# Performance work log

Measured on AMD Instinct MI355X. Metric: run time of the kernel, lower is better.

## Reference

```python
import jax, jax.numpy as jnp
import numpy as np
from jax import lax

# static config
P = 16          # patch_len
S = 8           # stride_base
MAX_OFF = 4.0


def setup_inputs() -> dict:
    key = jax.random.key(0)
    ks = jax.random.split(key, 7)
    B, L, N, A, D = 64, 512, 64, 64, 256
    x = jax.random.normal(ks[0], (B, L, N), dtype=jnp.float32)
    conv_w = jax.random.normal(ks[1], (32, N, 3), dtype=jnp.float32) * 0.05
    conv_b = jnp.zeros((32,), dtype=jnp.float32)
    lin_w = jax.random.normal(ks[2], (A, 32), dtype=jnp.float32) * 0.1
    lin_b = jnp.zeros((A,), dtype=jnp.float32)
    wp_w = jax.random.normal(ks[3], (D, P), dtype=jnp.float32) * 0.1
    wp_b = jnp.zeros((D,), dtype=jnp.float32)
    return {"x": x, "conv_w": conv_w, "conv_b": conv_b,
            "lin_w": lin_w, "lin_b": lin_b, "wp_w": wp_w, "wp_b": wp_b}


def _forward(x, conv_w, conv_b, lin_w, lin_b, wp_w, wp_b):
    B, L, N = x.shape
    A = lin_w.shape[0]
    D = wp_w.shape[0]
    z = jnp.transpose(x, (0, 2, 1))  # (B, N, L) -- channels = series

    # offset head: Conv1d(N->32, k=3, pad=1) -> ReLU -> global avg pool -> Linear(32->A)
    h = lax.conv_general_dilated(z, conv_w, window_strides=(1,),
                                 padding=[(1, 1)],
                                 dimension_numbers=("NCH", "OIH", "NCH"))
    h = jax.nn.relu(h + conv_b[None, :, None])      # (B, 32, L)
    pooled = jnp.mean(h, axis=-1)                    # (B, 32)
    delta = MAX_OFF * jnp.tanh(pooled @ lin_w.T + lin_b)  # (B, A)

    # sampling positions: anchor + offset + centered patch index, clamped to [0, L-1]
    anchors = jnp.arange(A, dtype=jnp.float32) * S
    pidx = jnp.arange(P, dtype=jnp.float32) - (P - 1) / 2.0
    xs = anchors[None, :, None] + delta[:, :, None] + pidx[None, None, :]  # (B, A, P)
    xs = jnp.clip(xs, 0.0, float(L - 1))

    # 1D bilinear gather (equivalent to grid_sample with y=0, border pad, align_corners=True)
    i0 = jnp.floor(xs).astype(jnp.int32)
    f = xs - i0.astype(xs.dtype)                     # (B, A, P)
    i1 = jnp.minimum(i0 + 1, L - 1)
    gather = jax.vmap(lambda zb, ib: zb[:, ib])      # (N,L),(A,P) -> (N,A,P)
    g0 = gather(z, i0)                               # (B, N, A, P)
    g1 = gather(z, i1)
    samp = g0 * (1.0 - f)[:, None] + g1 * f[:, None]  # (B, N, A, P)

    # patch projection W_P: (P -> D)
    out = jnp.einsum("bnap,dp->bnad", samp, wp_w) + wp_b  # (B, N, A, D)
    return out.reshape(B * N, A, D)


def reference(x, conv_w, conv_b, lin_w, lin_b, wp_w, wp_b):
    return _forward(x, conv_w, conv_b, lin_w, lin_b, wp_w, wp_b)
```

## Files before the change

kernel.cpp:

```cpp
#include <hip/hip_runtime.h>
#include <hip/hip_bf16.h>
#include <cmath>

#define BB 64
#define LL 512
#define NN 64
#define AA 64
#define PP 16
#define DD 256
#define MAX_OFF 4.0f
#define STRIDE_S 8

typedef __attribute__((ext_vector_type(8))) short short8_t;
typedef __attribute__((ext_vector_type(4))) float float4_t;

static __device__ __forceinline__ unsigned f2bf(float x) {
    union { float f; unsigned u; } v; v.f = x;
    return (v.u + 0x7FFFu + ((v.u >> 16) & 1u)) >> 16;
}

__global__ __launch_bounds__(256) void conv_pool_kernel(
    const float* __restrict__ x,
    const float* __restrict__ conv_w,
    const float* __restrict__ conv_b,
    float* __restrict__ pool_partial)
{
    const int c = blockIdx.x;
    const int b = blockIdx.y;
    const int t = threadIdx.x;

    __shared__ float4 wl[3 * 16 * 32];
    __shared__ float  xl[66 * 64];
    __shared__ float  red[8][32];

    for (int idx = t; idx < 1536; idx += 256) {
        int o  = idx & 31;
        int nv = (idx >> 5) & 15;
        int k  = idx >> 9;
        float4 v;
        v.x = conv_w[(o * 64 + nv * 4 + 0) * 3 + k];
        v.y = conv_w[(o * 64 + nv * 4 + 1) * 3 + k];
        v.z = conv_w[(o * 64 + nv * 4 + 2) * 3 + k];
        v.w = conv_w[(o * 64 + nv * 4 + 3) * 3 + k];
        wl[idx] = v;
    }

    const int base_row = c * 64 - 1;
    for (int idx = t; idx < 66 * 16; idx += 256) {
        int j  = idx >> 4;
        int nv = idx & 15;
        int row = base_row + j;
        float4 v = make_float4(0.f, 0.f, 0.f, 0.f);
        if (row >= 0 && row < LL)
            v = *reinterpret_cast<const float4*>(&x[((size_t)b * LL + row) * NN + nv * 4]);
        *reinterpret_cast<float4*>(&xl[j * 64 + nv * 4]) = v;
    }
    __syncthreads();

    const int o  = t & 31;
    const int lg = t >> 5;

    float s[8];
#pragma unroll
    for (int j = 0; j < 8; ++j) s[j] = 0.f;

#pragma unroll
    for (int nv = 0; nv < 16; ++nv) {
        float4 xv[10];
#pragma unroll
        for (int j = 0; j < 10; ++j)
            xv[j] = *reinterpret_cast<const float4*>(&xl[(lg * 8 + j) * 64 + nv * 4]);
#pragma unroll
        for (int k = 0; k < 3; ++k) {
            float4 w4 = wl[(k * 16 + nv) * 32 + o];
#pragma unroll
            for (int j = 0; j < 8; ++j) {
                s[j] = fmaf(xv[j + k].x, w4.x, s[j]);
                s[j] = fmaf(xv[j + k].y, w4.y, s[j]);
                s[j] = fmaf(xv[j + k].z, w4.z, s[j]);
                s[j] = fmaf(xv[j + k].w, w4.w, s[j]);
            }
        }
    }

    const float cb = conv_b[o];
    float part = 0.f;
#pragma unroll
    for (int j = 0; j < 8; ++j) part += fmaxf(s[j] + cb, 0.f);
    red[lg][o] = part;
    __syncthreads();

    if (t < 32) {
        float sum = 0.f;
#pragma unroll
        for (int g = 0; g < 8; ++g) sum += red[g][t];
        pool_partial[((size_t)b * 8 + c) * 32 + t] = sum;
    }
}

__global__ __launch_bounds__(64) void delta_kernel(
    const float* __restrict__ pool_partial,
    const float* __restrict__ lin_w,
    const float* __restrict__ lin_b,
    const float* __restrict__ wp_w,
    float* __restrict__ delta,
    unsigned short* __restrict__ wp16)
{
    const int b = blockIdx.x;
    const int t = threadIdx.x;
    __shared__ float pooled[32];

    if (t < 32) {
        float s = 0.f;
#pragma unroll
        for (int c = 0; c < 8; ++c) s += pool_partial[((size_t)b * 8 + c) * 32 + t];
        pooled[t] = s * (1.0f / 512.0f);
    }
    __syncthreads();

    float s = lin_b[t];
#pragma unroll
    for (int o = 0; o < 32; ++o) s = fmaf(pooled[o], lin_w[t * 32 + o], s);
    delta[b * AA + t] = MAX_OFF * tanhf(s);

    if (b == 0) {
        const float4* w4 = reinterpret_cast<const float4*>(wp_w);
        uint2* o2 = reinterpret_cast<uint2*>(wp16);
#pragma unroll
        for (int i = 0; i < 16; ++i) {
            float4 v = w4[i * 64 + t];
            uint2 pk;
            pk.x = f2bf(v.x) | (f2bf(v.y) << 16);
            pk.y = f2bf(v.z) | (f2bf(v.w) << 16);
            o2[i * 64 + t] = pk;
        }
    }
}

#define XR_STRIDE 68
#define SA_ST     24

__global__ __launch_bounds__(256) void patch_proj_kernel(
    const float* __restrict__ x,
    const unsigned short* __restrict__ wp16,
    const float* __restrict__ wp_b,
    const float* __restrict__ delta,
    float* __restrict__ out)
{
    const int a = blockIdx.x;
    const int b = blockIdx.y;
    const int t = threadIdx.x;
    const int lane = t & 63;
    const int w  = t >> 6;
    const int lg = lane >> 4;
    const int lr = lane & 15;

    __shared__ float          xr[17 * XR_STRIDE];
    __shared__ unsigned short sampA[64 * SA_ST];

    const float dlt  = delta[b * AA + a];
    const float base = (float)(a * STRIDE_S) - 7.5f + dlt;
    const int   r0   = (int)floorf(base);

    for (int idx = t; idx < 17 * 16; idx += 256) {
        int j  = idx >> 4;
        int nv = idx & 15;
        int row = max(0, min(LL - 1, r0 + j));
        float4 v = *reinterpret_cast<const float4*>(&x[((size_t)b * LL + row) * NN + nv * 4]);
        *reinterpret_cast<float4*>(&xr[j * XR_STRIDE + nv * 4]) = v;
    }

    short8_t afrag[4];
    float4_t acc[4][4];
    const short8_t zero8 = {0, 0, 0, 0, 0, 0, 0, 0};
#pragma unroll
    for (int i = 0; i < 4; ++i) {
        const int d = w * 64 + i * 16 + lr;
        short8_t v = *reinterpret_cast<const short8_t*>(&wp16[d * 16 + (lg & 1) * 8]);
        afrag[i] = (lg < 2) ? v : zero8;
        float4 bv = *reinterpret_cast<const float4*>(&wp_b[w * 64 + i * 16 + lg * 4]);
        float4_t c4 = {bv.x, bv.y, bv.z, bv.w};
#pragma unroll
        for (int s = 0; s < 4; ++s) acc[s][i] = c4;
    }
    __syncthreads();

    {
        const int pp  = t & 7;
        const int nr0 = t >> 3;
        float f_[2]; int j0_[2], j1_[2];
#pragma unroll
        for (int q = 0; q < 2; ++q) {
            int p = pp * 2 + q;
            float xs = base + (float)p;
            xs = fminf(fmaxf(xs, 0.f), (float)(LL - 1));
            int i0 = (int)floorf(xs);
            f_[q]  = xs - (float)i0;
            j0_[q] = i0 - r0;
            j1_[q] = min(i0 + 1, LL - 1) - r0;
        }
#pragma unroll
        for (int h = 0; h < 2; ++h) {
            int n = nr0 + 32 * h;
            unsigned pk = 0;
#pragma unroll
            for (int q = 0; q < 2; ++q) {
                float g0 = xr[j0_[q] * XR_STRIDE + n];
                float g1 = xr[j1_[q] * XR_STRIDE + n];
                float s  = g0 + f_[q] * (g1 - g0);
                pk |= f2bf(s) << (16 * q);
            }
            *reinterpret_cast<unsigned*>(&sampA[n * SA_ST + pp * 2]) = pk;
        }
    }
    __syncthreads();

    short8_t bfrag[4];
#pragma unroll
    for (int s = 0; s < 4; ++s)
        bfrag[s] = *reinterpret_cast<const short8_t*>(
            &sampA[(s * 16 + lr) * SA_ST + (lg & 1) * 8]);

#pragma unroll
    for (int s = 0; s < 4; ++s)
#pragma unroll
        for (int i = 0; i < 4; ++i)
            acc[s][i] = __builtin_amdgcn_mfma_f32_16x16x32_bf16(
                afrag[i], bfrag[s], acc[s][i], 0, 0, 0);

    const size_t ob = (((size_t)b * NN) * AA + a) * DD + w * 64 + lg * 4;
#pragma unroll
    for (int s = 0; s < 4; ++s) {
        const int n = s * 16 + lr;
        const size_t rb = ob + (size_t)n * (AA * DD);
#pragma unroll
        for (int i = 0; i < 4; ++i)
            *reinterpret_cast<float4_t*>(&out[rb + i * 16]) = acc[s][i];
    }
}

extern "C" void kernel_launch(void* const* d_in, const int* in_sizes, int n_in,
                              void* d_out, int out_size, void* d_ws, size_t ws_size,
                              hipStream_t stream)
{
    const float* x      = (const float*)d_in[0];
    const float* conv_w = (const float*)d_in[1];
    const float* conv_b = (const float*)d_in[2];
    const float* lin_w  = (const float*)d_in[3];
    const float* lin_b  = (const float*)d_in[4];
    const float* wp_w   = (const float*)d_in[5];
    const float* wp_b   = (const float*)d_in[6];
    float* out = (float*)d_out;

    float* pool_partial = (float*)d_ws;
    float* delta        = pool_partial + 16384;
    unsigned short* wp16 = (unsigned short*)(delta + 4096);

    conv_pool_kernel<<<dim3(8, BB), 256, 0, stream>>>(x, conv_w, conv_b, pool_partial);
    delta_kernel<<<BB, 64, 0, stream>>>(pool_partial, lin_w, lin_b, wp_w, delta, wp16);
    patch_proj_kernel<<<dim3(AA, BB), 256, 0, stream>>>(x, wp16, wp_b, delta, out);
}
```

Baseline: 65.52 us.

## Fuse delta computation into patch projection and process four anchors per block

Removes the separate delta kernel: each patch-projection block now reduces the pooled partials, computes tanh offsets for its anchors, and converts wp_w to bf16 in registers. Each block handles four anchors, sharing one larger x window (49 rows) and the weight fragments across them, with a quarter of the blocks. This drops a kernel launch and its dependency gap and amortises setup per block. The cost is redundant pooled/offset and weight-conversion work in every block, plus less parallelism. The 49-row window assumes offsets stay within ±4, which MAX_OFF guarantees.

```diff
diff --git a/kernel.cpp b/kernel.cpp
--- a/kernel.cpp
+++ b/kernel.cpp
@@ -98,144 +98,148 @@
     }
 }
 
-__global__ __launch_bounds__(64) void delta_kernel(
+#define AGRP 4
+#define XROWS 49
+#define XR_STRIDE 68
+#define SA_ST 24
+
+__global__ __launch_bounds__(256) void patch_proj_kernel(
+    const float* __restrict__ x,
+    const float* __restrict__ wp_w,
+    const float* __restrict__ wp_b,
     const float* __restrict__ pool_partial,
     const float* __restrict__ lin_w,
     const float* __restrict__ lin_b,
-    const float* __restrict__ wp_w,
-    float* __restrict__ delta,
-    unsigned short* __restrict__ wp16)
-{
-    const int b = blockIdx.x;
-    const int t = threadIdx.x;
-    __shared__ float pooled[32];
-
-    if (t < 32) {
-        float s = 0.f;
-#pragma unroll
-        for (int c = 0; c < 8; ++c) s += pool_partial[((size_t)b * 8 + c) * 32 + t];
-        pooled[t] = s * (1.0f / 512.0f);
-    }
-    __syncthreads();
-
-    float s = lin_b[t];
-#pragma unroll
-    for (int o = 0; o < 32; ++o) s = fmaf(pooled[o], lin_w[t * 32 + o], s);
-    delta[b * AA + t] = MAX_OFF * tanhf(s);
-
-    if (b == 0) {
-        const float4* w4 = reinterpret_cast<const float4*>(wp_w);
-        uint2* o2 = reinterpret_cast<uint2*>(wp16);
-#pragma unroll
-        for (int i = 0; i < 16; ++i) {
-            float4 v = w4[i * 64 + t];
-            uint2 pk;
-            pk.x = f2bf(v.x) | (f2bf(v.y) << 16);
-            pk.y = f2bf(v.z) | (f2bf(v.w) << 16);
-            o2[i * 64 + t] = pk;
-        }
-    }
-}
-
-#define XR_STRIDE 68
-#define SA_ST     24
-
-__global__ __launch_bounds__(256) void patch_proj_kernel(
-    const float* __restrict__ x,
-    const unsigned short* __restrict__ wp16,
-    const float* __restrict__ wp_b,
-    const float* __restrict__ delta,
     float* __restrict__ out)
 {
-    const int a = blockIdx.x;
-    const int b = blockIdx.y;
-    const int t = threadIdx.x;
+    const int a0 = blockIdx.x * AGRP;
+    const int b  = blockIdx.y;
+    const int t  = threadIdx.x;
     const int lane = t & 63;
     const int w  = t >> 6;
     const int lg = lane >> 4;
     const int lr = lane & 15;
 
-    __shared__ float          xr[17 * XR_STRIDE];
-    __shared__ unsigned short sampA[64 * SA_ST];
-
-    const float dlt  = delta[b * AA + a];
-    const float base = (float)(a * STRIDE_S) - 7.5f + dlt;
-    const int   r0   = (int)floorf(base);
-
-    for (int idx = t; idx < 17 * 16; idx += 256) {
+    __shared__ float          xr[XROWS * XR_STRIDE];
+    __shared__ unsigned short sampA[AGRP * 64 * SA_ST];
+    __shared__ float          pooled[32];
+    __shared__ float          bases[AGRP];
+
+    const int r_lo = a0 * 8 - 12;
+
+    for (int idx = t; idx < XROWS * 16; idx += 256) {
         int j  = idx >> 4;
         int nv = idx & 15;
-        int row = max(0, min(LL - 1, r0 + j));
+        int row = max(0, min(LL - 1, r_lo + j));
         float4 v = *reinterpret_cast<const float4*>(&x[((size_t)b * LL + row) * NN + nv * 4]);
         *reinterpret_cast<float4*>(&xr[j * XR_STRIDE + nv * 4]) = v;
     }
-
-    short8_t afrag[4];
-    float4_t acc[4][4];
-    const short8_t zero8 = {0, 0, 0, 0, 0, 0, 0, 0};
-#pragma unroll
-    for (int i = 0; i < 4; ++i) {
-        const int d = w * 64 + i * 16 + lr;
-        short8_t v = *reinterpret_cast<const short8_t*>(&wp16[d * 16 + (lg & 1) * 8]);
-        afrag[i] = (lg < 2) ? v : zero8;
-        float4 bv = *reinterpret_cast<const float4*>(&wp_b[w * 64 + i * 16 + lg * 4]);
-        float4_t c4 = {bv.x, bv.y, bv.z, bv.w};
-#pragma unroll
-        for (int s = 0; s < 4; ++s) acc[s][i] = c4;
+    if (t < 32) {
+        float s = 0.f;
+#pragma unroll
+        for (int c = 0; c < 8; ++c) s += pool_partial[((size_t)b * 8 + c) * 32 + t];
+        pooled[t] = s * (1.0f / 512.0f);
+    }
+    __syncthreads();
+
+    if (t < AGRP) {
+        const int a = a0 + t;
+        float s = lin_b[a];
+#pragma unroll
+        for (int o = 0; o < 32; ++o) s = fmaf(pooled[o], lin_w[a * 32 + o], s);
+        bases[t] = (float)(a * STRIDE_S) - 7.5f + MAX_OFF * tanhf(s);
     }
     __syncthreads();
 
     {
         const int pp  = t & 7;
         const int nr0 = t >> 3;
-        float f_[2]; int j0_[2], j1_[2];
-#pragma unroll
-        for (int q = 0; q < 2; ++q) {
-            int p = pp * 2 + q;
-            float xs = base + (float)p;
-            xs = fminf(fmaxf(xs, 0.f), (float)(LL - 1));
-            int i0 = (int)floorf(xs);
-            f_[q]  = xs - (float)i0;
-            j0_[q] = i0 - r0;
-            j1_[q] = min(i0 + 1, LL - 1) - r0;
-        }
-#pragma unroll
-        for (int h = 0; h < 2; ++h) {
-            int n = nr0 + 32 * h;
-            unsigned pk = 0;
+#pragma unroll
+        for (int al = 0; al < AGRP; ++al) {
+            const float base = bases[al];
+            float f_[2]; int j0_[2], j1_[2];
 #pragma unroll
             for (int q = 0; q < 2; ++q) {
-                float g0 = xr[j0_[q] * XR_STRIDE + n];
-                float g1 = xr[j1_[q] * XR_STRIDE + n];
-                float s  = g0 + f_[q] * (g1 - g0);
-                pk |= f2bf(s) << (16 * q);
+                int p = pp * 2 + q;
+                float xs = base + (float)p;
+                xs = fminf(fmaxf(xs, 0.f), (float)(LL - 1));
+                int i0 = (int)floorf(xs);
+                f_[q]  = xs - (float)i0;
+                j0_[q] = i0 - r_lo;
+                j1_[q] = min(i0 + 1, LL - 1) - r_lo;
             }
-            *reinterpret_cast<unsigned*>(&sampA[n * SA_ST + pp * 2]) = pk;
-        }
-    }
-    __syncthreads();
-
-    short8_t bfrag[4];
-#pragma unroll
-    for (int s = 0; s < 4; ++s)
-        bfrag[s] = *reinterpret_cast<const short8_t*>(
-            &sampA[(s * 16 + lr) * SA_ST + (lg & 1) * 8]);
-
-#pragma unroll
-    for (int s = 0; s < 4; ++s)
-#pragma unroll
-        for (int i = 0; i < 4; ++i)
-            acc[s][i] = __builtin_amdgcn_mfma_f32_16x16x32_bf16(
-                afrag[i], bfrag[s], acc[s][i], 0, 0, 0);
-
-    const size_t ob = (((size_t)b * NN) * AA + a) * DD + w * 64 + lg * 4;
-#pragma unroll
-    for (int s = 0; s < 4; ++s) {
-        const int n = s * 16 + lr;
-        const size_t rb = ob + (size_t)n * (AA * DD);
-#pragma unroll
-        for (int i = 0; i < 4; ++i)
-            *reinterpret_cast<float4_t*>(&out[rb + i * 16]) = acc[s][i];
+#pragma unroll
+            for (int h = 0; h < 2; ++h) {
+                int n = nr0 + 32 * h;
+                unsigned pk = 0;
+#pragma unroll
+                for (int q = 0; q < 2; ++q) {
+                    float g0 = xr[j0_[q] * XR_STRIDE + n];
+                    float g1 = xr[j1_[q] * XR_STRIDE + n];
+                    float s  = g0 + f_[q] * (g1 - g0);
+                    pk |= f2bf(s) << (16 * q);
+                }
+                *reinterpret_cast<unsigned*>(&sampA[(al * 64 + n) * SA_ST + pp * 2]) = pk;
+            }
+        }
+    }
+
+    short8_t afrag[4];
+    float4   bias4[4];
+    const short8_t zero8 = {0, 0, 0, 0, 0, 0, 0, 0};
+#pragma unroll
+    for (int i = 0; i < 4; ++i) {
+        const int d = w * 64 + i * 16 + lr;
+        short8_t v = zero8;
+        if (lg < 2) {
+            float4 w0 = *reinterpret_cast<const float4*>(&wp_w[d * 16 + lg * 8 + 0]);
+            float4 w1 = *reinterpret_cast<const float4*>(&wp_w[d * 16 + lg * 8 + 4]);
+            unsigned p0 = f2bf(w0.x) | (f2bf(w0.y) << 16);
+            unsigned p1 = f2bf(w0.z) | (f2bf(w0.w) << 16);
+            unsigned p2 = f2bf(w1.x) | (f2bf(w1.y) << 16);
+            unsigned p3 = f2bf(w1.z) | (f2bf(w1.w) << 16);
+            v[0] = (short)(p0 & 0xFFFF); v[1] = (short)(p0 >> 16);
+            v[2] = (short)(p1 & 0xFFFF); v[3] = (short)(p1 >> 16);
+            v[4] = (short)(p2 & 0xFFFF); v[5] = (short)(p2 >> 16);
+            v[6] = (short)(p3 & 0xFFFF); v[7] = (short)(p3 >> 16);
+        }
+        afrag[i] = v;
+        bias4[i] = *reinterpret_cast<const float4*>(&wp_b[w * 64 + i * 16 + lg * 4]);
+    }
+    __syncthreads();
+
+    const size_t ob0 = (((size_t)b * NN) * AA + a0) * DD + w * 64 + lg * 4;
+#pragma unroll
+    for (int al = 0; al < AGRP; ++al) {
+        short8_t bfrag[4];
+#pragma unroll
+        for (int s = 0; s < 4; ++s)
+            bfrag[s] = *reinterpret_cast<const short8_t*>(
+                &sampA[(al * 64 + s * 16 + lr) * SA_ST + (lg & 1) * 8]);
+
+        float4_t acc[4][4];
+#pragma unroll
+        for (int i = 0; i < 4; ++i) {
+            float4_t c4 = {bias4[i].x, bias4[i].y, bias4[i].z, bias4[i].w};
+#pragma unroll
+            for (int s = 0; s < 4; ++s) acc[s][i] = c4;
+        }
+#pragma unroll
+        for (int s = 0; s < 4; ++s)
+#pragma unroll
+            for (int i = 0; i < 4; ++i)
+                acc[s][i] = __builtin_amdgcn_mfma_f32_16x16x32_bf16(
+                    afrag[i], bfrag[s], acc[s][i], 0, 0, 0);
+
+        const size_t ob = ob0 + (size_t)al * DD;
+#pragma unroll
+        for (int s = 0; s < 4; ++s) {
+            const int n = s * 16 + lr;
+            const size_t rb = ob + (size_t)n * (AA * DD);
+#pragma unroll
+            for (int i = 0; i < 4; ++i)
+                *reinterpret_cast<float4_t*>(&out[rb + i * 16]) = acc[s][i];
+        }
     }
 }
 
@@ -253,10 +257,8 @@
     float* out = (float*)d_out;
 
     float* pool_partial = (float*)d_ws;
-    float* delta        = pool_partial + 16384;
-    unsigned short* wp16 = (unsigned short*)(delta + 4096);
 
     conv_pool_kernel<<<dim3(8, BB), 256, 0, stream>>>(x, conv_w, conv_b, pool_partial);
-    delta_kernel<<<BB, 64, 0, stream>>>(pool_partial, lin_w, lin_b, wp_w, delta, wp16);
-    patch_proj_kernel<<<dim3(AA, BB), 256, 0, stream>>>(x, wp16, wp_b, delta, out);
-}
+    patch_proj_kernel<<<dim3(AA / AGRP, BB), 256, 0, stream>>>(
+        x, wp_w, wp_b, pool_partial, lin_w, lin_b, out);
+}
```

After: 71.75 us. +9.5%, slower.

## Restructure patch projection to per-series blocks with contiguous output planes

Applied to the files above, without the earlier changes.

The patch projection kernel now assigns each block four series of one batch instead of one anchor. It loads the full length of those four series columns into shared memory and computes all 64 anchors. Each block therefore writes contiguous A×D planes of the output rather than strided rows spread across the whole output, which should improve write coalescing. The bf16 weight conversion moves from the delta kernel into a separate small kernel, adding one launch. The grid shrinks from 4096 to 1024 blocks, each doing four times the MFMA work serially.

```diff
diff --git a/kernel.cpp b/kernel.cpp
--- a/kernel.cpp
+++ b/kernel.cpp
@@ -102,9 +102,7 @@
     const float* __restrict__ pool_partial,
     const float* __restrict__ lin_w,
     const float* __restrict__ lin_b,
-    const float* __restrict__ wp_w,
-    float* __restrict__ delta,
-    unsigned short* __restrict__ wp16)
+    float* __restrict__ delta)
 {
     const int b = blockIdx.x;
     const int t = threadIdx.x;
@@ -122,120 +120,119 @@
 #pragma unroll
     for (int o = 0; o < 32; ++o) s = fmaf(pooled[o], lin_w[t * 32 + o], s);
     delta[b * AA + t] = MAX_OFF * tanhf(s);
-
-    if (b == 0) {
-        const float4* w4 = reinterpret_cast<const float4*>(wp_w);
-        uint2* o2 = reinterpret_cast<uint2*>(wp16);
-#pragma unroll
-        for (int i = 0; i < 16; ++i) {
-            float4 v = w4[i * 64 + t];
-            uint2 pk;
-            pk.x = f2bf(v.x) | (f2bf(v.y) << 16);
-            pk.y = f2bf(v.z) | (f2bf(v.w) << 16);
-            o2[i * 64 + t] = pk;
-        }
-    }
-}
-
-#define XR_STRIDE 68
-#define SA_ST     24
-
-__global__ __launch_bounds__(256) void patch_proj_kernel(
+}
+
+__global__ __launch_bounds__(256) void cvt_kernel(
+    const float* __restrict__ w, unsigned short* __restrict__ o)
+{
+    int i = blockIdx.x * 256 + threadIdx.x;
+    o[i] = (unsigned short)f2bf(w[i]);
+}
+
+#define CL_ST 516
+#define SA_ST 24
+
+__global__ __launch_bounds__(256) void patch_plane_kernel(
     const float* __restrict__ x,
     const unsigned short* __restrict__ wp16,
     const float* __restrict__ wp_b,
     const float* __restrict__ delta,
     float* __restrict__ out)
 {
-    const int a = blockIdx.x;
-    const int b = blockIdx.y;
-    const int t = threadIdx.x;
+    const int nq4 = blockIdx.x * 4;
+    const int b   = blockIdx.y;
+    const int t   = threadIdx.x;
     const int lane = t & 63;
     const int w  = t >> 6;
     const int lg = lane >> 4;
     const int lr = lane & 15;
 
-    __shared__ float          xr[17 * XR_STRIDE];
-    __shared__ unsigned short sampA[64 * SA_ST];
-
-    const float dlt  = delta[b * AA + a];
-    const float base = (float)(a * STRIDE_S) - 7.5f + dlt;
-    const int   r0   = (int)floorf(base);
-
-    for (int idx = t; idx < 17 * 16; idx += 256) {
-        int j  = idx >> 4;
-        int nv = idx & 15;
-        int row = max(0, min(LL - 1, r0 + j));
-        float4 v = *reinterpret_cast<const float4*>(&x[((size_t)b * LL + row) * NN + nv * 4]);
-        *reinterpret_cast<float4*>(&xr[j * XR_STRIDE + nv * 4]) = v;
+    __shared__ float          cols[4][CL_ST];
+    __shared__ unsigned short sampA[4][64 * SA_ST];
+    __shared__ float          dl[AA];
+
+    if (t < AA) dl[t] = delta[b * AA + t];
+    for (int idx = t; idx < LL; idx += 256) {
+        float4 v = *reinterpret_cast<const float4*>(&x[((size_t)b * LL + idx) * NN + nq4]);
+        cols[0][idx] = v.x;
+        cols[1][idx] = v.y;
+        cols[2][idx] = v.z;
+        cols[3][idx] = v.w;
     }
 
     short8_t afrag[4];
-    float4_t acc[4][4];
+    float4   bias4[4];
     const short8_t zero8 = {0, 0, 0, 0, 0, 0, 0, 0};
 #pragma unroll
     for (int i = 0; i < 4; ++i) {
         const int d = w * 64 + i * 16 + lr;
         short8_t v = *reinterpret_cast<const short8_t*>(&wp16[d * 16 + (lg & 1) * 8]);
         afrag[i] = (lg < 2) ? v : zero8;
-        float4 bv = *reinterpret_cast<const float4*>(&wp_b[w * 64 + i * 16 + lg * 4]);
-        float4_t c4 = {bv.x, bv.y, bv.z, bv.w};
-#pragma unroll
-        for (int s = 0; s < 4; ++s) acc[s][i] = c4;
+        bias4[i] = *reinterpret_cast<const float4*>(&wp_b[w * 64 + i * 16 + lg * 4]);
     }
     __syncthreads();
 
     {
-        const int pp  = t & 7;
-        const int nr0 = t >> 3;
-        float f_[2]; int j0_[2], j1_[2];
-#pragma unroll
-        for (int q = 0; q < 2; ++q) {
-            int p = pp * 2 + q;
-            float xs = base + (float)p;
+        const int aa = t >> 2;
+        const int pg = (t & 3) * 4;
+        const float base = (float)(aa * STRIDE_S) - 7.5f + dl[aa];
+        int i0_[4], i1_[4]; float f_[4];
+#pragma unroll
+        for (int q = 0; q < 4; ++q) {
+            float xs = base + (float)(pg + q);
             xs = fminf(fmaxf(xs, 0.f), (float)(LL - 1));
             int i0 = (int)floorf(xs);
             f_[q]  = xs - (float)i0;
-            j0_[q] = i0 - r0;
-            j1_[q] = min(i0 + 1, LL - 1) - r0;
-        }
-#pragma unroll
-        for (int h = 0; h < 2; ++h) {
-            int n = nr0 + 32 * h;
-            unsigned pk = 0;
-#pragma unroll
-            for (int q = 0; q < 2; ++q) {
-                float g0 = xr[j0_[q] * XR_STRIDE + n];
-                float g1 = xr[j1_[q] * XR_STRIDE + n];
-                float s  = g0 + f_[q] * (g1 - g0);
-                pk |= f2bf(s) << (16 * q);
+            i0_[q] = i0;
+            i1_[q] = min(i0 + 1, LL - 1);
+        }
+#pragma unroll
+        for (int j = 0; j < 4; ++j) {
+            float sv[4];
+#pragma unroll
+            for (int q = 0; q < 4; ++q) {
+                float g0 = cols[j][i0_[q]];
+                float g1 = cols[j][i1_[q]];
+                sv[q] = g0 + f_[q] * (g1 - g0);
             }
-            *reinterpret_cast<unsigned*>(&sampA[n * SA_ST + pp * 2]) = pk;
-        }
-    }
-    __syncthreads();
-
-    short8_t bfrag[4];
-#pragma unroll
-    for (int s = 0; s < 4; ++s)
-        bfrag[s] = *reinterpret_cast<const short8_t*>(
-            &sampA[(s * 16 + lr) * SA_ST + (lg & 1) * 8]);
-
-#pragma unroll
-    for (int s = 0; s < 4; ++s)
-#pragma unroll
-        for (int i = 0; i < 4; ++i)
-            acc[s][i] = __builtin_amdgcn_mfma_f32_16x16x32_bf16(
-                afrag[i], bfrag[s], acc[s][i], 0, 0, 0);
-
-    const size_t ob = (((size_t)b * NN) * AA + a) * DD + w * 64 + lg * 4;
-#pragma unroll
-    for (int s = 0; s < 4; ++s) {
-        const int n = s * 16 + lr;
-        const size_t rb = ob + (size_t)n * (AA * DD);
-#pragma unroll
-        for (int i = 0; i < 4; ++i)
-            *reinterpret_cast<float4_t*>(&out[rb + i * 16]) = acc[s][i];
+            uint2 pk;
+            pk.x = f2bf(sv[0]) | (f2bf(sv[1]) << 16);
+            pk.y = f2bf(sv[2]) | (f2bf(sv[3]) << 16);
+            *reinterpret_cast<uint2*>(&sampA[j][aa * SA_ST + pg]) = pk;
+        }
+    }
+    __syncthreads();
+
+#pragma unroll
+    for (int j = 0; j < 4; ++j) {
+        short8_t bfrag[4];
+#pragma unroll
+        for (int s = 0; s < 4; ++s)
+            bfrag[s] = *reinterpret_cast<const short8_t*>(
+                &sampA[j][(s * 16 + lr) * SA_ST + (lg & 1) * 8]);
+
+        float4_t acc[4][4];
+#pragma unroll
+        for (int i = 0; i < 4; ++i) {
+            float4_t c4 = {bias4[i].x, bias4[i].y, bias4[i].z, bias4[i].w};
+#pragma unroll
+            for (int s = 0; s < 4; ++s) acc[s][i] = c4;
+        }
+#pragma unroll
+        for (int s = 0; s < 4; ++s)
+#pragma unroll
+            for (int i = 0; i < 4; ++i)
+                acc[s][i] = __builtin_amdgcn_mfma_f32_16x16x32_bf16(
+                    afrag[i], bfrag[s], acc[s][i], 0, 0, 0);
+
+        const size_t pb = ((size_t)(b * NN + nq4 + j) * AA) * DD + w * 64 + lg * 4;
+#pragma unroll
+        for (int s = 0; s < 4; ++s) {
+            const size_t rb = pb + (size_t)(s * 16 + lr) * DD;
+#pragma unroll
+            for (int i = 0; i < 4; ++i)
+                *reinterpret_cast<float4_t*>(&out[rb + i * 16]) = acc[s][i];
+        }
     }
 }
 
@@ -257,6 +254,7 @@
     unsigned short* wp16 = (unsigned short*)(delta + 4096);
 
     conv_pool_kernel<<<dim3(8, BB), 256, 0, stream>>>(x, conv_w, conv_b, pool_partial);
-    delta_kernel<<<BB, 64, 0, stream>>>(pool_partial, lin_w, lin_b, wp_w, delta, wp16);
-    patch_proj_kernel<<<dim3(AA, BB), 256, 0, stream>>>(x, wp16, wp_b, delta, out);
-}
+    delta_kernel<<<BB, 64, 0, stream>>>(pool_partial, lin_w, lin_b, delta);
+    cvt_kernel<<<16, 256, 0, stream>>>(wp_w, wp16);
+    patch_plane_kernel<<<dim3(NN / 4, BB), 256, 0, stream>>>(x, wp16, wp_b, delta, out);
+}
```

New measurement: 72.82 us. +11.1%, slower.

## Compute bilinear samples per wave directly from global memory, removing block barriers

Applied to the files above, without the earlier changes.

The patch projection kernel no longer stages a 17-row x window in shared memory behind two block-wide barriers. Each wave now redundantly computes the full 64x16 bilinear sample tile, reading x directly from global memory, and writes it into a private column-major LDS buffer. It relies only on an lgkmcnt wait before reading the B fragments, since no other wave touches that buffer. This trades four times the sampling arithmetic and more global loads (mostly cache hits) for removing the __syncthreads stalls.

```diff
diff --git a/kernel.cpp b/kernel.cpp
--- a/kernel.cpp
+++ b/kernel.cpp
@@ -137,8 +137,7 @@
     }
 }
 
-#define XR_STRIDE 68
-#define SA_ST     24
+#define ST2 67
 
 __global__ __launch_bounds__(256) void patch_proj_kernel(
     const float* __restrict__ x,
@@ -155,20 +154,7 @@
     const int lg = lane >> 4;
     const int lr = lane & 15;
 
-    __shared__ float          xr[17 * XR_STRIDE];
-    __shared__ unsigned short sampA[64 * SA_ST];
-
-    const float dlt  = delta[b * AA + a];
-    const float base = (float)(a * STRIDE_S) - 7.5f + dlt;
-    const int   r0   = (int)floorf(base);
-
-    for (int idx = t; idx < 17 * 16; idx += 256) {
-        int j  = idx >> 4;
-        int nv = idx & 15;
-        int row = max(0, min(LL - 1, r0 + j));
-        float4 v = *reinterpret_cast<const float4*>(&x[((size_t)b * LL + row) * NN + nv * 4]);
-        *reinterpret_cast<float4*>(&xr[j * XR_STRIDE + nv * 4]) = v;
-    }
+    __shared__ unsigned sampCM[4][8 * ST2];
 
     short8_t afrag[4];
     float4_t acc[4][4];
@@ -183,43 +169,38 @@
 #pragma unroll
         for (int s = 0; s < 4; ++s) acc[s][i] = c4;
     }
-    __syncthreads();
-
-    {
-        const int pp  = t & 7;
-        const int nr0 = t >> 3;
-        float f_[2]; int j0_[2], j1_[2];
+
+    const float dlt  = delta[b * AA + a];
+    const float base = (float)(a * STRIDE_S) - 7.5f + dlt;
+    const float* xb  = x + (size_t)b * (LL * NN);
+    unsigned* sw = sampCM[w];
+#pragma unroll
+    for (int pq = 0; pq < 8; ++pq) {
+        unsigned pk = 0;
 #pragma unroll
         for (int q = 0; q < 2; ++q) {
-            int p = pp * 2 + q;
-            float xs = base + (float)p;
+            float xs = base + (float)(pq * 2 + q);
             xs = fminf(fmaxf(xs, 0.f), (float)(LL - 1));
-            int i0 = (int)floorf(xs);
-            f_[q]  = xs - (float)i0;
-            j0_[q] = i0 - r0;
-            j1_[q] = min(i0 + 1, LL - 1) - r0;
+            int   i0 = (int)floorf(xs);
+            float f  = xs - (float)i0;
+            int   i1 = min(i0 + 1, LL - 1);
+            float g0 = xb[i0 * NN + lane];
+            float g1 = xb[i1 * NN + lane];
+            pk |= f2bf(g0 + f * (g1 - g0)) << (16 * q);
         }
-#pragma unroll
-        for (int h = 0; h < 2; ++h) {
-            int n = nr0 + 32 * h;
-            unsigned pk = 0;
-#pragma unroll
-            for (int q = 0; q < 2; ++q) {
-                float g0 = xr[j0_[q] * XR_STRIDE + n];
-                float g1 = xr[j1_[q] * XR_STRIDE + n];
-                float s  = g0 + f_[q] * (g1 - g0);
-                pk |= f2bf(s) << (16 * q);
-            }
-            *reinterpret_cast<unsigned*>(&sampA[n * SA_ST + pp * 2]) = pk;
-        }
-    }
-    __syncthreads();
+        sw[pq * ST2 + lane] = pk;
+    }
+    asm volatile("s_waitcnt lgkmcnt(0)" ::: "memory");
 
     short8_t bfrag[4];
 #pragma unroll
-    for (int s = 0; s < 4; ++s)
-        bfrag[s] = *reinterpret_cast<const short8_t*>(
-            &sampA[(s * 16 + lr) * SA_ST + (lg & 1) * 8]);
+    for (int s = 0; s < 4; ++s) {
+        union { unsigned u[4]; short8_t s8; } uu;
+#pragma unroll
+        for (int j = 0; j < 4; ++j)
+            uu.u[j] = sw[((lg & 1) * 4 + j) * ST2 + s * 16 + lr];
+        bfrag[s] = uu.s8;
+    }
 
 #pragma unroll
     for (int s = 0; s < 4; ++s)
```

After: 78.90 us. 1.2x slower.
